# Performance work log

Measured on AMD Instinct MI355X. Metric: run time of the kernel, lower is better.

## Reference

```python
import math
import jax, jax.numpy as jnp
import numpy as np

B, L, D, H = 2, 2048, 1024, 16
KD = D // H


def setup_inputs() -> dict:
    key = jax.random.key(0)
    k1, k2, k3 = jax.random.split(key, 3)
    x = jax.random.normal(k1, (B, L, D), dtype=jnp.float32)
    wqkv = jax.random.normal(k2, (D, 3 * D), dtype=jnp.float32) * (1.0 / math.sqrt(D))
    wend = jax.random.normal(k3, (D, D), dtype=jnp.float32) * (1.0 / math.sqrt(D))
    return {"x": x, "wqkv": wqkv, "wend": wend}


def reference(x, wqkv, wend):
    b, l, d = x.shape
    qkv = jnp.einsum('bld,de->ble', x, wqkv)  # (B, L, 3D)
    q, k, v = jnp.split(qkv, 3, axis=-1)
    # Faithful to the torch module: reshape (B, L, D) -> (B, H, L, KD) directly.
    qh = q.reshape(b, H, l, KD)
    kh = k.reshape(b, H, l, KD)
    vh = v.reshape(b, H, l, KD)
    scores = jnp.einsum('bhqk,bhsk->bhqs', qh, kh) / math.sqrt(KD)  # (B, H, L, L)
    causal_mask = jnp.triu(jnp.ones((l, l), dtype=bool), k=1)
    scores = jnp.where(causal_mask, -jnp.inf, scores)
    probs = jax.nn.softmax(scores, axis=-1)
    attended = jnp.einsum('bhqs,bhsk->bhqk', probs, vh)  # (B, H, L, KD)
    concatted = attended.transpose(0, 2, 1, 3).reshape(b, l, d)
    return jnp.einsum('bld,de->ble', concatted, wend)
```

## Files before the change

kernel.cpp:

```cpp
#include <hip/hip_runtime.h>
#include <hip/hip_bf16.h>
#include <cstddef>
#include <cstdint>

#define L_SEQ   2048
#define D_MODEL 1024
#define NH      16
#define HKD     64
#define TD3     3072
#define NBATCH  2

typedef __attribute__((ext_vector_type(8))) short bf16x8;
typedef __attribute__((ext_vector_type(4))) float f32x4;

__device__ __forceinline__ unsigned short f2bf(float f) {
  unsigned int u = __float_as_uint(f);
  u += 0x7fffu + ((u >> 16) & 1u);
  return (unsigned short)(u >> 16);
}

__device__ __forceinline__ unsigned int pk2bf(float a, float b) {
  union { __hip_bfloat162 h; unsigned int u; } cv;
  cv.h = __float22bfloat162_rn(make_float2(a, b));
  return cv.u;
}

__device__ __forceinline__ void gll16(const void* g, void* l) {
  __builtin_amdgcn_global_load_lds(
      (const __attribute__((address_space(1))) unsigned int*)g,
      (__attribute__((address_space(3))) unsigned int*)l, 16, 0, 0);
}

__global__ __launch_bounds__(256)
void cvt_f32_bf16(const float* __restrict__ in, unsigned short* __restrict__ out) {
  const int i = blockIdx.x * 256 + threadIdx.x;
  const float4 a = ((const float4*)in)[2 * i];
  const float4 b = ((const float4*)in)[2 * i + 1];
  bf16x8 v;
  v[0] = (short)f2bf(a.x); v[1] = (short)f2bf(a.y);
  v[2] = (short)f2bf(a.z); v[3] = (short)f2bf(a.w);
  v[4] = (short)f2bf(b.x); v[5] = (short)f2bf(b.y);
  v[6] = (short)f2bf(b.z); v[7] = (short)f2bf(b.w);
  ((bf16x8*)out)[i] = v;
}

__global__ __launch_bounds__(256)
void transpose_cvt(const float* __restrict__ W, unsigned short* __restrict__ WT,
                   int K, int N) {
  __shared__ unsigned short T[64][68];
  const int t = threadIdx.x;
  const int n0 = blockIdx.x * 64, k0 = blockIdx.y * 64;
  const int cr = t >> 4, cc = (t & 15) * 4;
#pragma unroll
  for (int i = 0; i < 4; ++i) {
    const int k = cr + 16 * i;
    const float4 v = *(const float4*)(W + (size_t)(k0 + k) * N + n0 + cc);
    T[cc + 0][k] = f2bf(v.x); T[cc + 1][k] = f2bf(v.y);
    T[cc + 2][k] = f2bf(v.z); T[cc + 3][k] = f2bf(v.w);
  }
  __syncthreads();
#pragma unroll
  for (int i = 0; i < 4; ++i) {
    const int n = cr + 16 * i;
    ushort4 o;
    o.x = T[n][cc]; o.y = T[n][cc + 1]; o.z = T[n][cc + 2]; o.w = T[n][cc + 3];
    *(ushort4*)(WT + (size_t)(n0 + n) * K + k0 + cc) = o;
  }
}

template <typename OUT>
__device__ __forceinline__ OUT cvt_out(float f);
template <> __device__ __forceinline__ float cvt_out<float>(float f) { return f; }
template <> __device__ __forceinline__ unsigned short cvt_out<unsigned short>(float f) { return f2bf(f); }

template <typename OUT>
__global__ __launch_bounds__(256)
void gemm_bf16(const unsigned short* __restrict__ A,
               const unsigned short* __restrict__ Bt,
               OUT* __restrict__ C, int M, int N, int K) {
  __shared__ unsigned short As[128 * 64];
  __shared__ unsigned short Bs[128 * 64];
  const int t = threadIdx.x, w = t >> 6, lane = t & 63;
  const int lg = lane >> 4, lq = lane & 15;

  const int nwg = gridDim.x * gridDim.y;
  int bid = blockIdx.y * gridDim.x + blockIdx.x;
  bid = (bid & 7) * (nwg >> 3) + (bid >> 3);
  const int m0 = (bid / gridDim.x) * 128, n0 = (bid % gridDim.x) * 128;
  const int wr = w >> 1, wc = w & 1;

  f32x4 acc[4][4];
#pragma unroll
  for (int a = 0; a < 4; ++a)
#pragma unroll
    for (int b = 0; b < 4; ++b) acc[a][b] = (f32x4)0.f;

  for (int k0 = 0; k0 < K; k0 += 64) {
    __syncthreads();
#pragma unroll
    for (int i = 0; i < 4; ++i) {
      const int c = 256 * i + t;
      const int row = c >> 3, cc = (c & 7) * 8;
      gll16(A + (size_t)(m0 + row) * K + k0 + cc,
            (char*)As + (256 * i + 64 * w) * 16);
      gll16(Bt + (size_t)(n0 + row) * K + k0 + cc,
            (char*)Bs + (256 * i + 64 * w) * 16);
    }
    __syncthreads();
#pragma unroll
    for (int ks = 0; ks < 2; ++ks) {
      bf16x8 af[4], bfr[4];
#pragma unroll
      for (int mf = 0; mf < 4; ++mf)
        af[mf] = *(const bf16x8*)((const char*)As +
                   (wr * 64 + mf * 16 + lq) * 128 + ks * 64 + lg * 16);
#pragma unroll
      for (int nf = 0; nf < 4; ++nf)
        bfr[nf] = *(const bf16x8*)((const char*)Bs +
                   (wc * 64 + nf * 16 + lq) * 128 + ks * 64 + lg * 16);
#pragma unroll
      for (int mf = 0; mf < 4; ++mf)
#pragma unroll
        for (int nf = 0; nf < 4; ++nf)
          acc[mf][nf] = __builtin_amdgcn_mfma_f32_16x16x32_bf16(
              af[mf], bfr[nf], acc[mf][nf], 0, 0, 0);
    }
  }

#pragma unroll
  for (int mf = 0; mf < 4; ++mf)
#pragma unroll
    for (int nf = 0; nf < 4; ++nf) {
      const int col = n0 + wc * 64 + nf * 16 + lq;
#pragma unroll
      for (int r = 0; r < 4; ++r) {
        const int row = m0 + wr * 64 + mf * 16 + lg * 4 + r;
        C[(size_t)row * N + col] = cvt_out<OUT>(acc[mf][nf][r]);
      }
    }
}

__device__ __forceinline__ size_t head_row(int part, int b, int h, int s) {
  return ((size_t)(b * L_SEQ + h * 128 + (s >> 4))) * TD3 +
         (size_t)part * D_MODEL + (size_t)(s & 15) * HKD;
}

__global__ __launch_bounds__(256)
void transpose_v(const unsigned short* __restrict__ qkv,
                 unsigned short* __restrict__ vT) {
  __shared__ unsigned short T[64][68];
  const int t = threadIdx.x;
  const int kt = blockIdx.x, bh = blockIdx.y, b = bh >> 4, h = bh & 15;
  const int s0 = kt * 64;
  const int sr = t >> 4, c4 = (t & 15) * 4;
#pragma unroll
  for (int i = 0; i < 4; ++i) {
    const int s = sr + 16 * i;
    const ushort4 v = *(const ushort4*)(qkv + head_row(2, b, h, s0 + s) + c4);
    T[c4 + 0][s] = v.x; T[c4 + 1][s] = v.y;
    T[c4 + 2][s] = v.z; T[c4 + 3][s] = v.w;
  }
  __syncthreads();
#pragma unroll
  for (int i = 0; i < 4; ++i) {
    const int d = sr + 16 * i;
    ushort4 o;
    o.x = T[d][c4]; o.y = T[d][c4 + 1]; o.z = T[d][c4 + 2]; o.w = T[d][c4 + 3];
    *(ushort4*)(vT + ((size_t)(bh * 64 + d)) * L_SEQ + s0 + c4) = o;
  }
}

#define QK_SCALE 0.18033688011112043f

__global__ __launch_bounds__(512)
void attn_mfma(const unsigned short* __restrict__ qkv,
               const unsigned short* __restrict__ vT,
               unsigned short* __restrict__ concat) {
  __shared__ unsigned short Ks[2][64 * 64];
  __shared__ unsigned short Vs[2][64 * 64];
  __shared__ unsigned short Pl[8][16][72];

  const int t = threadIdx.x, w = t >> 6, lane = t & 63;
  const int lg = lane >> 4, lq = lane & 15;

  const int bid = blockIdx.x;
  const int xcd = bid & 7, idx = bid >> 3;
  const int bh = xcd + 8 * (idx & 3);
  const int pair = idx >> 2;
  const int b = bh >> 4, h = bh & 15;

  const int srow = t >> 3;
  const int swz = ((t & 7) ^ (srow & 7)) * 8;
  const size_t kSrc = head_row(1, b, h, srow) + swz;
  const size_t vSrc = ((size_t)(bh * 64 + srow)) * L_SEQ + swz;
  char* const kDst = (char*)&Ks[0][0] + w * 1024;
  char* const vDst = (char*)&Vs[0][0] + w * 1024;

  for (int pass = 0; pass < 2; ++pass) {
    const int qt = pass ? pair : 15 - pair;
    const int q0 = qt * 128;
    const int qrow = q0 + w * 16 + lq;

    bf16x8 qf[2];
    {
      const size_t qb = head_row(0, b, h, qrow) + lg * 8;
      qf[0] = *(const bf16x8*)(qkv + qb);
      qf[1] = *(const bf16x8*)(qkv + qb + 32);
#pragma unroll
      for (int s = 0; s < 2; ++s)
#pragma unroll
        for (int j = 0; j < 8; ++j) {
          const float f =
              __uint_as_float(((unsigned int)(unsigned short)qf[s][j]) << 16);
          qf[s][j] = (short)f2bf(f * QK_SCALE);
        }
    }

    f32x4 o[4];
#pragma unroll
    for (int mf = 0; mf < 4; ++mf) o[mf] = (f32x4)0.f;
    float mrun = -1e30f, lrun = 0.f;

    const int ktmax = 2 * qt + 1;

    __syncthreads();
    gll16(qkv + kSrc, kDst);
    gll16(vT + vSrc, vDst);

    for (int kt = 0; kt <= ktmax; ++kt) {
      const int k0 = kt * 64;
      const int cur = kt & 1;
      __syncthreads();

      if (kt < ktmax) {
        gll16(qkv + kSrc + (size_t)(k0 + 64) * 192, kDst + (1 - cur) * 8192);
        gll16(vT + vSrc + (size_t)(k0 + 64), vDst + (1 - cur) * 8192);
      }

      if (k0 > q0 + w * 16 + 15) continue;

      const char* kb = (const char*)&Ks[cur][0];
      const char* vb = (const char*)&Vs[cur][0];

      f32x4 s[4];
#pragma unroll
      for (int mf = 0; mf < 4; ++mf) s[mf] = (f32x4)0.f;
      __builtin_amdgcn_s_setprio(1);
#pragma unroll
      for (int ks = 0; ks < 2; ++ks) {
        bf16x8 kf[4];
#pragma unroll
        for (int mf = 0; mf < 4; ++mf) {
          const int key = mf * 16 + lq;
          const int chunk = (lg + 4 * ks) ^ (key & 7);
          kf[mf] = *(const bf16x8*)(kb + key * 128 + chunk * 16);
        }
#pragma unroll
        for (int mf = 0; mf < 4; ++mf)
          s[mf] = __builtin_amdgcn_mfma_f32_16x16x32_bf16(kf[mf], qf[ks], s[mf], 0, 0, 0);
      }
      __builtin_amdgcn_s_setprio(0);

      float sv[16];
      if (k0 + 63 > qrow - lq) {
#pragma unroll
        for (int mf = 0; mf < 4; ++mf)
#pragma unroll
          for (int r = 0; r < 4; ++r) {
            float x = s[mf][r];
            if (k0 + mf * 16 + lg * 4 + r > qrow) x = -1e30f;
            sv[mf * 4 + r] = x;
          }
      } else {
#pragma unroll
        for (int mf = 0; mf < 4; ++mf)
#pragma unroll
          for (int r = 0; r < 4; ++r) sv[mf * 4 + r] = s[mf][r];
      }
      float t0 = fmaxf(fmaxf(sv[0], sv[1]), fmaxf(sv[2], sv[3]));
      float t1 = fmaxf(fmaxf(sv[4], sv[5]), fmaxf(sv[6], sv[7]));
      float t2 = fmaxf(fmaxf(sv[8], sv[9]), fmaxf(sv[10], sv[11]));
      float t3 = fmaxf(fmaxf(sv[12], sv[13]), fmaxf(sv[14], sv[15]));
      float tmax = fmaxf(fmaxf(t0, t1), fmaxf(t2, t3));
      tmax = fmaxf(tmax, __shfl_xor(tmax, 16));
      tmax = fmaxf(tmax, __shfl_xor(tmax, 32));

      if (!__all(tmax - mrun <= 8.f)) {
        const float mnew = fmaxf(mrun, tmax);
        const float sc = __builtin_amdgcn_exp2f(mrun - mnew);
        lrun *= sc;
#pragma unroll
        for (int mf = 0; mf < 4; ++mf) {
          o[mf][0] *= sc; o[mf][1] *= sc; o[mf][2] *= sc; o[mf][3] *= sc;
        }
        mrun = mnew;
      }

      float rs = 0.f;
#pragma unroll
      for (int mf = 0; mf < 4; ++mf) {
        const float p0 = __builtin_amdgcn_exp2f(sv[mf * 4 + 0] - mrun);
        const float p1 = __builtin_amdgcn_exp2f(sv[mf * 4 + 1] - mrun);
        const float p2 = __builtin_amdgcn_exp2f(sv[mf * 4 + 2] - mrun);
        const float p3 = __builtin_amdgcn_exp2f(sv[mf * 4 + 3] - mrun);
        rs += (p0 + p1) + (p2 + p3);
        uint2 pk;
        pk.x = pk2bf(p0, p1);
        pk.y = pk2bf(p2, p3);
        *(uint2*)&Pl[w][lq][mf * 16 + lg * 4] = pk;
      }
      rs += __shfl_xor(rs, 16);
      rs += __shfl_xor(rs, 32);
      lrun += rs;

      __builtin_amdgcn_s_setprio(1);
#pragma unroll
      for (int ks = 0; ks < 2; ++ks) {
        const bf16x8 pf = *(const bf16x8*)&Pl[w][lq][ks * 32 + lg * 8];
        bf16x8 vf[4];
#pragma unroll
        for (int mf = 0; mf < 4; ++mf) {
          const int d = mf * 16 + lq;
          const int chunk = (lg + 4 * ks) ^ (d & 7);
          vf[mf] = *(const bf16x8*)(vb + d * 128 + chunk * 16);
        }
#pragma unroll
        for (int mf = 0; mf < 4; ++mf)
          o[mf] = __builtin_amdgcn_mfma_f32_16x16x32_bf16(vf[mf], pf, o[mf], 0, 0, 0);
      }
      __builtin_amdgcn_s_setprio(0);
    }

    const float inv = 1.f / lrun;
#pragma unroll
    for (int mf = 0; mf < 4; ++mf) {
      uint2 ov;
      ov.x = pk2bf(o[mf][0] * inv, o[mf][1] * inv);
      ov.y = pk2bf(o[mf][2] * inv, o[mf][3] * inv);
      *(uint2*)(concat + (size_t)(b * L_SEQ + qrow) * D_MODEL + h * HKD +
                mf * 16 + lg * 4) = ov;
    }
  }
}

extern "C" void kernel_launch(void* const* d_in, const int* in_sizes, int n_in,
                              void* d_out, int out_size, void* d_ws, size_t ws_size,
                              hipStream_t stream) {
  const float* x    = (const float*)d_in[0];
  const float* wqkv = (const float*)d_in[1];
  const float* wend = (const float*)d_in[2];
  float* out = (float*)d_out;

  char* ws = (char*)d_ws;
  unsigned short* qkv   = (unsigned short*)(ws);
  unsigned short* xb    = (unsigned short*)(ws + 25165824);
  unsigned short* wqkvT = (unsigned short*)(ws + 33554432);
  unsigned short* wendT = (unsigned short*)(ws + 39845888);
  unsigned short* cat   = (unsigned short*)(ws + 41943040);
  unsigned short* vT    = xb;

  cvt_f32_bf16<<<2048, 256, 0, stream>>>(x, xb);
  transpose_cvt<<<dim3(48, 16), 256, 0, stream>>>(wqkv, wqkvT, 1024, 3072);
  transpose_cvt<<<dim3(16, 16), 256, 0, stream>>>(wend, wendT, 1024, 1024);

  gemm_bf16<unsigned short><<<dim3(24, 32), 256, 0, stream>>>(
      xb, wqkvT, qkv, 4096, 3072, 1024);
  transpose_v<<<dim3(32, 32), 256, 0, stream>>>(qkv, vT);
  attn_mfma<<<256, 512, 0, stream>>>(qkv, vT, cat);
  gemm_bf16<float><<<dim3(8, 32), 256, 0, stream>>>(
      cat, wendT, out, 4096, 1024, 1024);
}
```

Baseline: 212.4 us.

## Double-buffer GEMM LDS tiles and XOR-swizzle to avoid bank conflicts

The bf16 GEMM now keeps two LDS buffers for the A and B tiles. It issues the async global-to-LDS loads for the next K tile before computing on the current one, using a single barrier per iteration instead of two. The tile columns are also XOR-swizzled by row on both the store and the fragment read, to cut LDS bank conflicts on the 16-byte fragment loads. This doubles LDS use per block, which may lower occupancy, and it relies on the barrier waiting for the outstanding async loads.

```diff
diff --git a/kernel.cpp b/kernel.cpp
--- a/kernel.cpp
+++ b/kernel.cpp
@@ -78,8 +78,8 @@
 void gemm_bf16(const unsigned short* __restrict__ A,
                const unsigned short* __restrict__ Bt,
                OUT* __restrict__ C, int M, int N, int K) {
-  __shared__ unsigned short As[128 * 64];
-  __shared__ unsigned short Bs[128 * 64];
+  __shared__ unsigned short As[2][128 * 64];
+  __shared__ unsigned short Bs[2][128 * 64];
   const int t = threadIdx.x, w = t >> 6, lane = t & 63;
   const int lg = lane >> 4, lq = lane & 15;
 
@@ -89,35 +89,53 @@
   const int m0 = (bid / gridDim.x) * 128, n0 = (bid % gridDim.x) * 128;
   const int wr = w >> 1, wc = w & 1;
 
+  const int srow = t >> 3;
+  const int ssw = ((t & 7) ^ (srow & 7)) * 8;
+  const size_t aSrc = (size_t)(m0 + srow) * K + ssw;
+  const size_t bSrc = (size_t)(n0 + srow) * K + ssw;
+
+  auto STAGE = [&](int buf, int k0) {
+#pragma unroll
+    for (int i = 0; i < 4; ++i) {
+      gll16(A + aSrc + (size_t)(32 * i) * K + k0,
+            (char*)&As[buf][0] + (256 * i + 64 * w) * 16);
+      gll16(Bt + bSrc + (size_t)(32 * i) * K + k0,
+            (char*)&Bs[buf][0] + (256 * i + 64 * w) * 16);
+    }
+  };
+
   f32x4 acc[4][4];
 #pragma unroll
   for (int a = 0; a < 4; ++a)
 #pragma unroll
     for (int b = 0; b < 4; ++b) acc[a][b] = (f32x4)0.f;
 
-  for (int k0 = 0; k0 < K; k0 += 64) {
+  STAGE(0, 0);
+
+  const int KT = K >> 6;
+  for (int kt = 0; kt < KT; ++kt) {
+    const int cur = kt & 1;
     __syncthreads();
-#pragma unroll
-    for (int i = 0; i < 4; ++i) {
-      const int c = 256 * i + t;
-      const int row = c >> 3, cc = (c & 7) * 8;
-      gll16(A + (size_t)(m0 + row) * K + k0 + cc,
-            (char*)As + (256 * i + 64 * w) * 16);
-      gll16(Bt + (size_t)(n0 + row) * K + k0 + cc,
-            (char*)Bs + (256 * i + 64 * w) * 16);
-    }
-    __syncthreads();
+
+    if (kt + 1 < KT) STAGE(cur ^ 1, (kt + 1) << 6);
+
+    const char* ab = (const char*)&As[cur][0];
+    const char* bb = (const char*)&Bs[cur][0];
 #pragma unroll
     for (int ks = 0; ks < 2; ++ks) {
       bf16x8 af[4], bfr[4];
 #pragma unroll
-      for (int mf = 0; mf < 4; ++mf)
-        af[mf] = *(const bf16x8*)((const char*)As +
-                   (wr * 64 + mf * 16 + lq) * 128 + ks * 64 + lg * 16);
-#pragma unroll
-      for (int nf = 0; nf < 4; ++nf)
-        bfr[nf] = *(const bf16x8*)((const char*)Bs +
-                   (wc * 64 + nf * 16 + lq) * 128 + ks * 64 + lg * 16);
+      for (int mf = 0; mf < 4; ++mf) {
+        const int row = wr * 64 + mf * 16 + lq;
+        af[mf] = *(const bf16x8*)(ab + row * 128 +
+                                  (((ks << 2) + lg) ^ (lq & 7)) * 16);
+      }
+#pragma unroll
+      for (int nf = 0; nf < 4; ++nf) {
+        const int row = wc * 64 + nf * 16 + lq;
+        bfr[nf] = *(const bf16x8*)(bb + row * 128 +
+                                   (((ks << 2) + lg) ^ (lq & 7)) * 16);
+      }
 #pragma unroll
       for (int mf = 0; mf < 4; ++mf)
 #pragma unroll
```

Measured after the change: 194.3 us. -8.5%, faster.
